# Kernel optimization log

Measured on AMD Instinct MI355X. Metric: run time of the kernel, lower is better.

Reference implementation:

```python
import jax, jax.numpy as jnp
import numpy as np

N_NODES = 50000
N_EDGES = 600000
N_GRAPHS = 500
HID = 128
N_LAYERS = 3
N_CLASSES = 10


def setup_inputs() -> dict:
    key = jax.random.key(0)
    ks = jax.random.split(key, 10)
    x = jax.random.normal(ks[0], (N_NODES, HID), dtype=jnp.float32)
    edge_attr = jax.random.normal(ks[1], (N_EDGES, 4), dtype=jnp.float32)
    edge_index = jax.random.randint(ks[2], (2, N_EDGES), 0, N_NODES, dtype=jnp.int32)
    batch = jnp.sort(jax.random.randint(ks[3], (N_NODES,), 0, N_GRAPHS, dtype=jnp.int32))
    s = 1.0 / np.sqrt(HID)
    Wl = jax.random.normal(ks[4], (N_LAYERS, HID, HID), dtype=jnp.float32) * s
    bl = jax.random.normal(ks[5], (N_LAYERS, HID), dtype=jnp.float32) * s
    Wr = jax.random.normal(ks[6], (N_LAYERS, HID, HID), dtype=jnp.float32) * s
    W1 = jax.random.normal(ks[7], (HID, HID), dtype=jnp.float32) * s
    b1 = jnp.zeros((HID,), dtype=jnp.float32)
    W2 = jax.random.normal(ks[8], (N_CLASSES, HID), dtype=jnp.float32) * s
    b2 = jnp.zeros((N_CLASSES,), dtype=jnp.float32)
    return {"x": x, "edge_attr": edge_attr, "edge_index": edge_index, "batch": batch,
            "Wl": Wl, "bl": bl, "Wr": Wr, "W1": W1, "b1": b1, "W2": W2, "b2": b2}


def _sage_conv(x, src, dst, Wl_i, bl_i, Wr_i):
    # mean aggregation of source-node features at target nodes (PyG SAGEConv)
    msg_sum = jax.ops.segment_sum(x[src], dst, num_segments=N_NODES)  # [N, H]
    cnt = jax.ops.segment_sum(jnp.ones((src.shape[0],), x.dtype), dst, num_segments=N_NODES)
    mean = msg_sum / jnp.maximum(cnt, 1.0)[:, None]
    return mean @ Wl_i.T + bl_i + x @ Wr_i.T


def reference(x, edge_attr, edge_index, batch, Wl, bl, Wr, W1, b1, W2, b2):
    # edge_attr is ignored by SAGEConv
    src, dst = edge_index[0], edge_index[1]
    for i in range(N_LAYERS):
        x = jax.nn.relu(_sage_conv(x, src, dst, Wl[i], bl[i], Wr[i]))
    # global_add_pool over graphs
    g = jax.ops.segment_sum(x, batch, num_segments=N_GRAPHS)  # [G, H]
    g = jax.nn.relu(g)
    # dropout p=0.5 is identity at inference
    h = jax.nn.relu(g @ W1.T + b1)
    logits = h @ W2.T + b2
    return jax.nn.log_softmax(logits, axis=1)
```

## Files before the change

### kernel.cpp

```cpp
#include <hip/hip_runtime.h>
#include <math.h>

#define HID 128
#define NCLS 10
#define MAXDEG 32
#define TROWS 32
#define MSP 136

typedef __attribute__((ext_vector_type(8))) short frag8;
typedef __attribute__((ext_vector_type(8))) unsigned short u16x8;
typedef __attribute__((ext_vector_type(4))) float f32x4;

static __device__ __forceinline__ float relu_f(float v) { return v > 0.f ? v : 0.f; }

static __device__ __forceinline__ unsigned short f2bf(float f) {
    unsigned int u = __float_as_uint(f);
    u += 0x7fffu + ((u >> 16) & 1u);
    return (unsigned short)(u >> 16);
}
static __device__ __forceinline__ float bf2f(unsigned short u) {
    return __uint_as_float(((unsigned int)u) << 16);
}

static __device__ __forceinline__ void gld_lds16(const void* g, void* l) {
    __builtin_amdgcn_global_load_lds((const __attribute__((address_space(1))) unsigned int*)g,
                                     (__attribute__((address_space(3))) unsigned int*)l,
                                     16, 0, 0);
}

static __device__ __forceinline__ void conv4(const float* __restrict__ in,
                                             unsigned short* __restrict__ out, int i) {
    float4 v = *(const float4*)&in[i * 4];
    ushort4 o;
    o.x = f2bf(v.x); o.y = f2bf(v.y); o.z = f2bf(v.z); o.w = f2bf(v.w);
    *(ushort4*)&out[i * 4] = o;
}

__global__ __launch_bounds__(256) void prep_kernel(const float* __restrict__ x, unsigned short* __restrict__ xb, int nx4,
                                                   const float* __restrict__ Wl, unsigned short* __restrict__ wlb, int nwl4,
                                                   const float* __restrict__ Wr, unsigned short* __restrict__ wrb, int nwr4,
                                                   int* __restrict__ deg, int ndeg4,
                                                   uint4* __restrict__ colp, int ncol8, unsigned int zpat,
                                                   uint4* __restrict__ zp0, uint4* __restrict__ zp1,
                                                   uint4* __restrict__ zp2, int nz8) {
    int i = blockIdx.x * blockDim.x + threadIdx.x;
    if (i < nx4) { conv4(x, xb, i); return; }
    i -= nx4;
    if (i < nwl4) { conv4(Wl, wlb, i); return; }
    i -= nwl4;
    if (i < nwr4) { conv4(Wr, wrb, i); return; }
    i -= nwr4;
    if (i < ndeg4) { *(int4*)&deg[i * 4] = make_int4(0, 0, 0, 0); return; }
    i -= ndeg4;
    if (i < ncol8) { colp[i] = make_uint4(zpat, zpat, zpat, zpat); return; }
    i -= ncol8;
    if (i < nz8) { zp0[i] = make_uint4(0, 0, 0, 0); return; }
    i -= nz8;
    if (i < nz8) { zp1[i] = make_uint4(0, 0, 0, 0); return; }
    i -= nz8;
    if (i < nz8) zp2[i] = make_uint4(0, 0, 0, 0);
}

__global__ void fill_kernel(const int* __restrict__ src, const int* __restrict__ dst,
                            int* __restrict__ deg, unsigned short* __restrict__ col, int nE) {
    int e = blockIdx.x * blockDim.x + threadIdx.x;
    if (e < nE) {
        int d = dst[e];
        int p = atomicAdd(&deg[d], 1);
        if (p < MAXDEG) col[(long)d * MAXDEG + p] = (unsigned short)src[e];
    }
}

__global__ __launch_bounds__(256, 3) void sage_kernel(const unsigned short* __restrict__ Xb,
                                                      const int* __restrict__ deg,
                                                      const unsigned short* __restrict__ col,
                                                      const unsigned short* __restrict__ Wlb,
                                                      const unsigned short* __restrict__ Wrb,
                                                      const float* __restrict__ bl,
                                                      unsigned short* __restrict__ Yb, int nN) {
    __shared__ unsigned short ms[TROWS * MSP];
    __shared__ unsigned short stg[4 * 4096];

    const int r0 = blockIdx.x * TROWS;
    const int lane = threadIdx.x & 63;
    const int wave = threadIdx.x >> 6;
    const int grp4 = lane >> 4;
    const int l16 = lane & 15;
    const int fo = l16 * 8;
    unsigned short* stg_w = &stg[wave * 4096];

#pragma unroll
    for (int set = 0; set < 2; ++set) {
        const int nl = wave * 8 + set * 4 + grp4;
        const int n = r0 + nl;
        const int d = min(deg[n], MAXDEG);
        const unsigned short* cp = col + (long)n * MAXDEG;
        const int il = cp[l16];
        const int ih = cp[16 + l16];

        float acc[8] = {0, 0, 0, 0, 0, 0, 0, 0};

#pragma unroll
        for (int c = 0; c < 4; ++c) {
            const bool act = (c * 8 < d);
            if (act) {
                asm volatile("s_waitcnt lgkmcnt(0)" ::: "memory");
#pragma unroll
                for (int k = 0; k < 8; ++k) {
                    const int slot = c * 8 + k;
                    const int idx = (slot < 16) ? __shfl(il, slot, 16) : __shfl(ih, slot - 16, 16);
                    gld_lds16(Xb + (long)idx * HID + fo, stg_w + k * 512);
                }
#pragma unroll
                for (int k = 0; k < 8; ++k) {
                    asm volatile("s_waitcnt vmcnt(%0)" ::"i"(7 - k) : "memory");
                    u16x8 v = *(const u16x8*)&stg_w[k * 512 + lane * 8];
#pragma unroll
                    for (int j = 0; j < 8; ++j) acc[j] += bf2f(v[j]);
                }
            }
        }

        const float inv = 1.f / fmaxf((float)d, 1.f);
        u16x8 o;
#pragma unroll
        for (int j = 0; j < 8; ++j) o[j] = f2bf(acc[j] * inv);
        *(u16x8*)&ms[nl * MSP + fo] = o;
    }
    __syncthreads();

    const int l15 = lane & 15;
    const int quad = lane >> 4;
    const int wr = wave & 1;
    const int wc = wave >> 1;

    f32x4 acc[4];
#pragma unroll
    for (int ct = 0; ct < 4; ++ct) acc[ct] = (f32x4){0.f, 0.f, 0.f, 0.f};

#pragma unroll
    for (int ks = 0; ks < HID; ks += 32) {
        const int lrow = wr * 16 + l15;
        frag8 aM = *(const frag8*)&ms[lrow * MSP + ks + quad * 8];
        frag8 aX = *(const frag8*)&Xb[(long)(r0 + lrow) * HID + ks + quad * 8];
#pragma unroll
        for (int ct = 0; ct < 4; ++ct) {
            const long nrow = wc * 64 + ct * 16 + l15;
            frag8 bL = *(const frag8*)&Wlb[nrow * HID + ks + quad * 8];
            frag8 bR = *(const frag8*)&Wrb[nrow * HID + ks + quad * 8];
            acc[ct] = __builtin_amdgcn_mfma_f32_16x16x32_bf16(aM, bL, acc[ct], 0, 0, 0);
            acc[ct] = __builtin_amdgcn_mfma_f32_16x16x32_bf16(aX, bR, acc[ct], 0, 0, 0);
        }
    }

#pragma unroll
    for (int ct = 0; ct < 4; ++ct) {
        const int gc = wc * 64 + ct * 16 + l15;
        const float bb = bl[gc];
#pragma unroll
        for (int reg = 0; reg < 4; ++reg) {
            const int gm = r0 + wr * 16 + quad * 4 + reg;
            if (gm < nN) {
                const float v = relu_f(acc[ct][reg] + bb);
                Yb[(long)gm * HID + gc] = f2bf(v);
            }
        }
    }
}

__global__ __launch_bounds__(128) void poolmlp_kernel(const unsigned short* __restrict__ xb,
                                                      const int* __restrict__ batch, int nN,
                                                      const float* __restrict__ W1,
                                                      const float* __restrict__ b1,
                                                      const float* __restrict__ W2,
                                                      const float* __restrict__ b2,
                                                      float* __restrict__ out) {
    __shared__ float gs[HID];
    __shared__ float hs[HID];
    __shared__ float ls[NCLS];
    __shared__ float red[2];
    int gid = blockIdx.x;
    int j = threadIdx.x;

    int lo = 0, hi = nN;
    while (lo < hi) { int mid = (lo + hi) >> 1; if (batch[mid] < gid) lo = mid + 1; else hi = mid; }
    int s = lo;
    hi = nN;
    while (lo < hi) { int mid = (lo + hi) >> 1; if (batch[mid] < gid + 1) lo = mid + 1; else hi = mid; }
    int e = lo;

    float a0 = 0.f, a1 = 0.f, a2 = 0.f, a3 = 0.f;
    int n = s;
    for (; n + 4 <= e; n += 4) {
        a0 += bf2f(xb[(long)n * HID + j]);
        a1 += bf2f(xb[(long)(n + 1) * HID + j]);
        a2 += bf2f(xb[(long)(n + 2) * HID + j]);
        a3 += bf2f(xb[(long)(n + 3) * HID + j]);
    }
    for (; n < e; ++n) a0 += bf2f(xb[(long)n * HID + j]);
    gs[j] = relu_f((a0 + a1) + (a2 + a3));
    __syncthreads();

    float acc = b1[j];
#pragma unroll 8
    for (int k = 0; k < HID; ++k) acc += gs[k] * W1[j * HID + k];
    hs[j] = relu_f(acc);
    __syncthreads();
    if (j < NCLS) {
        float lg = b2[j];
#pragma unroll 8
        for (int k = 0; k < HID; ++k) lg += hs[k] * W2[j * HID + k];
        ls[j] = lg;
    }
    __syncthreads();
    if (j == 0) {
        float m = ls[0];
        for (int c = 1; c < NCLS; ++c) m = fmaxf(m, ls[c]);
        float sum = 0.f;
        for (int c = 0; c < NCLS; ++c) sum += expf(ls[c] - m);
        red[0] = m;
        red[1] = logf(sum);
    }
    __syncthreads();
    if (j < NCLS) out[gid * NCLS + j] = ls[j] - red[0] - red[1];
}


extern "C" void kernel_launch(void* const* d_in, const int* in_sizes, int n_in,
                              void* d_out, int out_size, void* d_ws, size_t ws_size,
                              hipStream_t stream) {
    const float* x_in  = (const float*)d_in[0];
    const int*   eidx  = (const int*)d_in[2];
    const int*   batch = (const int*)d_in[3];
    const float* Wl    = (const float*)d_in[4];
    const float* bl    = (const float*)d_in[5];
    const float* Wr    = (const float*)d_in[6];
    const float* W1    = (const float*)d_in[7];
    const float* b1    = (const float*)d_in[8];
    const float* W2    = (const float*)d_in[9];
    const float* b2    = (const float*)d_in[10];
    float* out = (float*)d_out;

    const int nN = in_sizes[0] / HID;
    const int nE = in_sizes[2] / 2;
    const int nG = out_size / NCLS;
    const int nWl = in_sizes[4];
    const int nWr = in_sizes[6];
    const int nNp = (nN + TROWS - 1) & ~(TROWS - 1);
    const int nTiles = nNp / TROWS;
    const int nRows = nNp + 8;

    const int* src = eidx;
    const int* dst = eidx + nE;

    char* p = (char*)d_ws;
    auto carve = [&](size_t bytes) {
        char* r = p;
        p += (bytes + 255) & ~(size_t)255;
        return r;
    };
    unsigned short* xb  = (unsigned short*)carve((size_t)nRows * HID * 2);
    unsigned short* yb0 = (unsigned short*)carve((size_t)nRows * HID * 2);
    unsigned short* yb1 = (unsigned short*)carve((size_t)nRows * HID * 2);
    unsigned short* wlb = (unsigned short*)carve((size_t)nWl * 2);
    unsigned short* wrb = (unsigned short*)carve((size_t)nWr * 2);
    int*   deg = (int*)carve((size_t)nNp * 4);
    unsigned short* col = (unsigned short*)carve((size_t)nNp * MAXDEG * 2);
    (void)ws_size; (void)n_in;

    const int nx4 = nN * HID / 4, nwl4 = nWl / 4, nwr4 = nWr / 4;
    const int ndeg4 = (nNp + 3) / 4;
    const int ncol8 = nNp * MAXDEG / 8;
    const int nzrows = nNp + 1 - nN;
    const int nz8 = nzrows * HID / 8;
    const unsigned int zpat = (unsigned int)nNp | ((unsigned int)nNp << 16);
    const int prep_total = nx4 + nwl4 + nwr4 + ndeg4 + ncol8 + 3 * nz8;
    prep_kernel<<<(prep_total + 255) / 256, 256, 0, stream>>>(
        x_in, xb, nx4, Wl, wlb, nwl4, Wr, wrb, nwr4, deg, ndeg4,
        (uint4*)col, ncol8, zpat,
        (uint4*)(xb + (size_t)nN * HID), (uint4*)(yb0 + (size_t)nN * HID),
        (uint4*)(yb1 + (size_t)nN * HID), nz8);

    fill_kernel<<<(nE + 255) / 256, 256, 0, stream>>>(src, dst, deg, col, nE);

    const unsigned short* xcur = xb;
    unsigned short* bufs[2] = {yb0, yb1};
    for (int l = 0; l < 3; ++l) {
        sage_kernel<<<nTiles, 256, 0, stream>>>(
            xcur, deg, col,
            wlb + (size_t)l * HID * HID, wrb + (size_t)l * HID * HID,
            bl + (size_t)l * HID, bufs[l & 1], nN);
        xcur = bufs[l & 1];
    }

    poolmlp_kernel<<<nG, 128, 0, stream>>>(xcur, batch, nN, W1, b1, W2, b2, out);
}
```

Measured before the change: 321.0 us.

## Double-buffer neighbor gather in 4-row chunks across both node sets

Restructures the mean-aggregation gather into a double-buffered software pipeline. Neighbor rows are fetched in chunks of 4 into two alternating LDS buffers, with the next chunk issued while the current one is accumulated. The chunk count is now set by the wave-wide maximum degree, rounded to multiples of 4 rather than 8, and both node sets are flattened into one loop. The aim is to hide global-load latency and cut wasted fetches for low-degree nodes. The cost is more registers (two accumulators) and extra wait/branch logic per chunk.

After: 427.2 us. 33.1% more time.

```diff
diff --git a/kernel.cpp b/kernel.cpp
--- a/kernel.cpp
+++ b/kernel.cpp
@@ -79,7 +79,7 @@
                                                       const float* __restrict__ bl,
                                                       unsigned short* __restrict__ Yb, int nN) {
     __shared__ unsigned short ms[TROWS * MSP];
-    __shared__ unsigned short stg[4 * 4096];
+    __shared__ unsigned short stg[4 * 2 * 2048];
 
     const int r0 = blockIdx.x * TROWS;
     const int lane = threadIdx.x & 63;
@@ -89,43 +89,83 @@
     const int fo = l16 * 8;
     unsigned short* stg_w = &stg[wave * 4096];
 
-#pragma unroll
-    for (int set = 0; set < 2; ++set) {
-        const int nl = wave * 8 + set * 4 + grp4;
-        const int n = r0 + nl;
-        const int d = min(deg[n], MAXDEG);
-        const unsigned short* cp = col + (long)n * MAXDEG;
-        const int il = cp[l16];
-        const int ih = cp[16 + l16];
-
-        float acc[8] = {0, 0, 0, 0, 0, 0, 0, 0};
-
-#pragma unroll
-        for (int c = 0; c < 4; ++c) {
-            const bool act = (c * 8 < d);
-            if (act) {
-                asm volatile("s_waitcnt lgkmcnt(0)" ::: "memory");
-#pragma unroll
-                for (int k = 0; k < 8; ++k) {
-                    const int slot = c * 8 + k;
-                    const int idx = (slot < 16) ? __shfl(il, slot, 16) : __shfl(ih, slot - 16, 16);
-                    gld_lds16(Xb + (long)idx * HID + fo, stg_w + k * 512);
+    const int n0 = r0 + wave * 8 + grp4;
+    const int n1 = n0 + 4;
+    const int d0 = min(deg[n0], MAXDEG);
+    const int d1 = min(deg[n1], MAXDEG);
+    const unsigned short* cp0 = col + (long)n0 * MAXDEG;
+    const unsigned short* cp1 = col + (long)n1 * MAXDEG;
+    const int il0 = cp0[l16], ih0 = cp0[16 + l16];
+    const int il1 = cp1[l16], ih1 = cp1[16 + l16];
+
+    int m0 = d0, m1 = d1;
+    m0 = max(m0, __shfl_xor(m0, 16)); m0 = max(m0, __shfl_xor(m0, 32));
+    m1 = max(m1, __shfl_xor(m1, 16)); m1 = max(m1, __shfl_xor(m1, 32));
+    const int nc0 = __builtin_amdgcn_readfirstlane((m0 + 3) >> 2);
+    const int ncT = nc0 + __builtin_amdgcn_readfirstlane((m1 + 3) >> 2);
+
+    float acc0[8] = {0, 0, 0, 0, 0, 0, 0, 0};
+    float acc1[8] = {0, 0, 0, 0, 0, 0, 0, 0};
+
+    auto issue = [&](int t) {
+        const int s = (t >= nc0) ? 1 : 0;
+        const int c = t - (s ? nc0 : 0);
+        const int iv = s ? ((c < 4) ? il1 : ih1) : ((c < 4) ? il0 : ih0);
+        const int sbase = (c < 4) ? c * 4 : c * 4 - 16;
+        unsigned short* sb = stg_w + (t & 1) * 2048;
+#pragma unroll
+        for (int k = 0; k < 4; ++k) {
+            const int idx = __shfl(iv, sbase + k, 16);
+            gld_lds16(Xb + (long)idx * HID + fo, sb + k * 512);
+        }
+    };
+
+    if (ncT > 0) {
+        issue(0);
+        if (ncT > 1) issue(1);
+        for (int t = 0; t < ncT; ++t) {
+            if (t + 1 < ncT) {
+                asm volatile("s_waitcnt vmcnt(4)" ::: "memory");
+            } else {
+                asm volatile("s_waitcnt vmcnt(0)" ::: "memory");
+            }
+            __builtin_amdgcn_sched_barrier(0);
+            const unsigned short* sb = stg_w + (t & 1) * 2048;
+            if (t < nc0) {
+#pragma unroll
+                for (int k = 0; k < 4; ++k) {
+                    u16x8 v = *(const u16x8*)&sb[k * 512 + lane * 8];
+#pragma unroll
+                    for (int j = 0; j < 8; ++j) acc0[j] += bf2f(v[j]);
                 }
-#pragma unroll
-                for (int k = 0; k < 8; ++k) {
-                    asm volatile("s_waitcnt vmcnt(%0)" ::"i"(7 - k) : "memory");
-                    u16x8 v = *(const u16x8*)&stg_w[k * 512 + lane * 8];
-#pragma unroll
-                    for (int j = 0; j < 8; ++j) acc[j] += bf2f(v[j]);
+            } else {
+#pragma unroll
+                for (int k = 0; k < 4; ++k) {
+                    u16x8 v = *(const u16x8*)&sb[k * 512 + lane * 8];
+#pragma unroll
+                    for (int j = 0; j < 8; ++j) acc1[j] += bf2f(v[j]);
                 }
             }
+            if (t + 2 < ncT) {
+                asm volatile("s_waitcnt lgkmcnt(0)" ::: "memory");
+                __builtin_amdgcn_sched_barrier(0);
+                issue(t + 2);
+            }
         }
-
-        const float inv = 1.f / fmaxf((float)d, 1.f);
-        u16x8 o;
-#pragma unroll
-        for (int j = 0; j < 8; ++j) o[j] = f2bf(acc[j] * inv);
-        *(u16x8*)&ms[nl * MSP + fo] = o;
+    }
+
+    {
+        const int nl0 = wave * 8 + grp4;
+        const float inv0 = 1.f / fmaxf((float)d0, 1.f);
+        u16x8 o0;
+#pragma unroll
+        for (int j = 0; j < 8; ++j) o0[j] = f2bf(acc0[j] * inv0);
+        *(u16x8*)&ms[nl0 * MSP + fo] = o0;
+        const float inv1 = 1.f / fmaxf((float)d1, 1.f);
+        u16x8 o1;
+#pragma unroll
+        for (int j = 0; j < 8; ++j) o1[j] = f2bf(acc1[j] * inv1);
+        *(u16x8*)&ms[(nl0 + 4) * MSP + fo] = o1;
     }
     __syncthreads();
 
```

## Gather neighbor features in FP8 copy and double rows per block

Applied to the files above, without the earlier changes.

Keeps an extra FP8 copy of node features, written in prep and by the first two layers, and gathers neighbor rows from it with direct vector loads. This replaces the LDS-staged bf16 global_load_lds path and halves gather bytes. TROWS doubles to 64, so each wave computes two 16-row MFMA tiles and reuses the weight fragments. The trade-off is lower precision in the mean aggregation, extra byte-wide FP8 stores in the epilogue, and fewer blocks in the grid.

Result: faster. 266.6 us (median of 2 runs) (-17.0%).

```diff
diff --git a/kernel.cpp b/kernel.cpp
--- a/kernel.cpp
+++ b/kernel.cpp
@@ -4,11 +4,12 @@
 #define HID 128
 #define NCLS 10
 #define MAXDEG 32
-#define TROWS 32
+#define TROWS 64
 #define MSP 136
 
 typedef __attribute__((ext_vector_type(8))) short frag8;
 typedef __attribute__((ext_vector_type(8))) unsigned short u16x8;
+typedef __attribute__((ext_vector_type(2))) unsigned int u32x2;
 typedef __attribute__((ext_vector_type(4))) float f32x4;
 
 static __device__ __forceinline__ float relu_f(float v) { return v > 0.f ? v : 0.f; }
@@ -22,10 +23,21 @@
     return __uint_as_float(((unsigned int)u) << 16);
 }
 
-static __device__ __forceinline__ void gld_lds16(const void* g, void* l) {
-    __builtin_amdgcn_global_load_lds((const __attribute__((address_space(1))) unsigned int*)g,
-                                     (__attribute__((address_space(3))) unsigned int*)l,
-                                     16, 0, 0);
+static __device__ __forceinline__ unsigned int f2fp8x4(float a, float b, float c, float d) {
+    int w = __builtin_amdgcn_cvt_pk_fp8_f32(a, b, 0, false);
+    w = __builtin_amdgcn_cvt_pk_fp8_f32(c, d, w, true);
+    return (unsigned int)w;
+}
+static __device__ __forceinline__ unsigned char f2fp8(float v) {
+    return (unsigned char)(__builtin_amdgcn_cvt_pk_fp8_f32(v, v, 0, false) & 0xff);
+}
+static __device__ __forceinline__ void f8acc(unsigned int w0, unsigned int w1, float* acc) {
+    auto p0 = __builtin_amdgcn_cvt_pk_f32_fp8((int)w0, false);
+    auto p1 = __builtin_amdgcn_cvt_pk_f32_fp8((int)w0, true);
+    auto p2 = __builtin_amdgcn_cvt_pk_f32_fp8((int)w1, false);
+    auto p3 = __builtin_amdgcn_cvt_pk_f32_fp8((int)w1, true);
+    acc[0] += p0[0]; acc[1] += p0[1]; acc[2] += p1[0]; acc[3] += p1[1];
+    acc[4] += p2[0]; acc[5] += p2[1]; acc[6] += p3[0]; acc[7] += p3[1];
 }
 
 static __device__ __forceinline__ void conv4(const float* __restrict__ in,
@@ -36,15 +48,25 @@
     *(ushort4*)&out[i * 4] = o;
 }
 
-__global__ __launch_bounds__(256) void prep_kernel(const float* __restrict__ x, unsigned short* __restrict__ xb, int nx4,
+__global__ __launch_bounds__(256) void prep_kernel(const float* __restrict__ x, unsigned short* __restrict__ xb,
+                                                   unsigned int* __restrict__ xf8w, int nx4,
                                                    const float* __restrict__ Wl, unsigned short* __restrict__ wlb, int nwl4,
                                                    const float* __restrict__ Wr, unsigned short* __restrict__ wrb, int nwr4,
                                                    int* __restrict__ deg, int ndeg4,
                                                    uint4* __restrict__ colp, int ncol8, unsigned int zpat,
                                                    uint4* __restrict__ zp0, uint4* __restrict__ zp1,
-                                                   uint4* __restrict__ zp2, int nz8) {
+                                                   uint4* __restrict__ zp2, int nz8,
+                                                   uint4* __restrict__ zf0, uint4* __restrict__ zf1,
+                                                   uint4* __restrict__ zf2) {
     int i = blockIdx.x * blockDim.x + threadIdx.x;
-    if (i < nx4) { conv4(x, xb, i); return; }
+    if (i < nx4) {
+        float4 v = *(const float4*)&x[i * 4];
+        ushort4 o;
+        o.x = f2bf(v.x); o.y = f2bf(v.y); o.z = f2bf(v.z); o.w = f2bf(v.w);
+        *(ushort4*)&xb[i * 4] = o;
+        xf8w[i] = f2fp8x4(v.x, v.y, v.z, v.w);
+        return;
+    }
     i -= nx4;
     if (i < nwl4) { conv4(Wl, wlb, i); return; }
     i -= nwl4;
@@ -58,7 +80,13 @@
     i -= nz8;
     if (i < nz8) { zp1[i] = make_uint4(0, 0, 0, 0); return; }
     i -= nz8;
-    if (i < nz8) zp2[i] = make_uint4(0, 0, 0, 0);
+    if (i < nz8) { zp2[i] = make_uint4(0, 0, 0, 0); return; }
+    i -= nz8;
+    if (i < 8) { zf0[i] = make_uint4(0, 0, 0, 0); return; }
+    i -= 8;
+    if (i < 8) { zf1[i] = make_uint4(0, 0, 0, 0); return; }
+    i -= 8;
+    if (i < 8) zf2[i] = make_uint4(0, 0, 0, 0);
 }
 
 __global__ void fill_kernel(const int* __restrict__ src, const int* __restrict__ dst,
@@ -72,84 +100,101 @@
 }
 
 __global__ __launch_bounds__(256, 3) void sage_kernel(const unsigned short* __restrict__ Xb,
+                                                      const unsigned char* __restrict__ Xf8,
                                                       const int* __restrict__ deg,
                                                       const unsigned short* __restrict__ col,
                                                       const unsigned short* __restrict__ Wlb,
                                                       const unsigned short* __restrict__ Wrb,
                                                       const float* __restrict__ bl,
-                                                      unsigned short* __restrict__ Yb, int nN) {
+                                                      unsigned short* __restrict__ Yb,
+                                                      unsigned char* __restrict__ Yf8,
+                                                      int wr8, int nN) {
     __shared__ unsigned short ms[TROWS * MSP];
-    __shared__ unsigned short stg[4 * 4096];
 
     const int r0 = blockIdx.x * TROWS;
+
+    {
+        const int grp = threadIdx.x >> 4;
+        const int l16 = threadIdx.x & 15;
+        const int fo8 = l16 * 8;
+        const long fo = (long)l16 * 8;
+
+        for (int i = 0; i < 4; ++i) {
+            const int nl = grp * 4 + i;
+            const int n = r0 + nl;
+            const int d = min(deg[n], MAXDEG);
+            const unsigned short* cp = col + (long)n * MAXDEG;
+
+            float acc[8] = {0, 0, 0, 0, 0, 0, 0, 0};
+
+            if (d > 0) {
+                u16x8 iv0 = *(const u16x8*)&cp[0];
+                u16x8 iv1 = *(const u16x8*)&cp[8];
+                u32x2 q[16];
+#pragma unroll
+                for (int k = 0; k < 8; ++k)
+                    q[k] = *(const u32x2*)&Xf8[(long)iv0[k] * HID + fo8];
+#pragma unroll
+                for (int k = 0; k < 8; ++k)
+                    q[8 + k] = *(const u32x2*)&Xf8[(long)iv1[k] * HID + fo8];
+#pragma unroll
+                for (int k = 0; k < 16; ++k) f8acc(q[k][0], q[k][1], acc);
+
+                if (d > 16) {
+                    u16x8 iv2 = *(const u16x8*)&cp[16];
+                    u16x8 iv3 = *(const u16x8*)&cp[24];
+#pragma unroll
+                    for (int k = 0; k < 8; ++k)
+                        q[k] = *(const u32x2*)&Xf8[(long)iv2[k] * HID + fo8];
+#pragma unroll
+                    for (int k = 0; k < 8; ++k)
+                        q[8 + k] = *(const u32x2*)&Xf8[(long)iv3[k] * HID + fo8];
+#pragma unroll
+                    for (int k = 0; k < 16; ++k) f8acc(q[k][0], q[k][1], acc);
+                }
+            }
+
+            const float inv = 1.f / fmaxf((float)d, 1.f);
+            u16x8 o;
+#pragma unroll
+            for (int j = 0; j < 8; ++j) o[j] = f2bf(acc[j] * inv);
+            *(u16x8*)&ms[nl * MSP + fo] = o;
+        }
+    }
+    __syncthreads();
+
     const int lane = threadIdx.x & 63;
     const int wave = threadIdx.x >> 6;
-    const int grp4 = lane >> 4;
-    const int l16 = lane & 15;
-    const int fo = l16 * 8;
-    unsigned short* stg_w = &stg[wave * 4096];
-
-#pragma unroll
-    for (int set = 0; set < 2; ++set) {
-        const int nl = wave * 8 + set * 4 + grp4;
-        const int n = r0 + nl;
-        const int d = min(deg[n], MAXDEG);
-        const unsigned short* cp = col + (long)n * MAXDEG;
-        const int il = cp[l16];
-        const int ih = cp[16 + l16];
-
-        float acc[8] = {0, 0, 0, 0, 0, 0, 0, 0};
-
-#pragma unroll
-        for (int c = 0; c < 4; ++c) {
-            const bool act = (c * 8 < d);
-            if (act) {
-                asm volatile("s_waitcnt lgkmcnt(0)" ::: "memory");
-#pragma unroll
-                for (int k = 0; k < 8; ++k) {
-                    const int slot = c * 8 + k;
-                    const int idx = (slot < 16) ? __shfl(il, slot, 16) : __shfl(ih, slot - 16, 16);
-                    gld_lds16(Xb + (long)idx * HID + fo, stg_w + k * 512);
-                }
-#pragma unroll
-                for (int k = 0; k < 8; ++k) {
-                    asm volatile("s_waitcnt vmcnt(%0)" ::"i"(7 - k) : "memory");
-                    u16x8 v = *(const u16x8*)&stg_w[k * 512 + lane * 8];
-#pragma unroll
-                    for (int j = 0; j < 8; ++j) acc[j] += bf2f(v[j]);
-                }
-            }
-        }
-
-        const float inv = 1.f / fmaxf((float)d, 1.f);
-        u16x8 o;
-#pragma unroll
-        for (int j = 0; j < 8; ++j) o[j] = f2bf(acc[j] * inv);
-        *(u16x8*)&ms[nl * MSP + fo] = o;
-    }
-    __syncthreads();
-
     const int l15 = lane & 15;
     const int quad = lane >> 4;
     const int wr = wave & 1;
     const int wc = wave >> 1;
 
-    f32x4 acc[4];
-#pragma unroll
-    for (int ct = 0; ct < 4; ++ct) acc[ct] = (f32x4){0.f, 0.f, 0.f, 0.f};
+    f32x4 acc[2][4];
+#pragma unroll
+    for (int rt = 0; rt < 2; ++rt)
+#pragma unroll
+        for (int ct = 0; ct < 4; ++ct) acc[rt][ct] = (f32x4){0.f, 0.f, 0.f, 0.f};
 
 #pragma unroll
     for (int ks = 0; ks < HID; ks += 32) {
-        const int lrow = wr * 16 + l15;
-        frag8 aM = *(const frag8*)&ms[lrow * MSP + ks + quad * 8];
-        frag8 aX = *(const frag8*)&Xb[(long)(r0 + lrow) * HID + ks + quad * 8];
+        frag8 aM[2], aX[2];
+#pragma unroll
+        for (int rt = 0; rt < 2; ++rt) {
+            const int lrow = wr * 32 + rt * 16 + l15;
+            aM[rt] = *(const frag8*)&ms[lrow * MSP + ks + quad * 8];
+            aX[rt] = *(const frag8*)&Xb[(long)(r0 + lrow) * HID + ks + quad * 8];
+        }
 #pragma unroll
         for (int ct = 0; ct < 4; ++ct) {
             const long nrow = wc * 64 + ct * 16 + l15;
             frag8 bL = *(const frag8*)&Wlb[nrow * HID + ks + quad * 8];
             frag8 bR = *(const frag8*)&Wrb[nrow * HID + ks + quad * 8];
-            acc[ct] = __builtin_amdgcn_mfma_f32_16x16x32_bf16(aM, bL, acc[ct], 0, 0, 0);
-            acc[ct] = __builtin_amdgcn_mfma_f32_16x16x32_bf16(aX, bR, acc[ct], 0, 0, 0);
+#pragma unroll
+            for (int rt = 0; rt < 2; ++rt) {
+                acc[rt][ct] = __builtin_amdgcn_mfma_f32_16x16x32_bf16(aM[rt], bL, acc[rt][ct], 0, 0, 0);
+                acc[rt][ct] = __builtin_amdgcn_mfma_f32_16x16x32_bf16(aX[rt], bR, acc[rt][ct], 0, 0, 0);
+            }
         }
     }
 
@@ -158,11 +203,15 @@
         const int gc = wc * 64 + ct * 16 + l15;
         const float bb = bl[gc];
 #pragma unroll
-        for (int reg = 0; reg < 4; ++reg) {
-            const int gm = r0 + wr * 16 + quad * 4 + reg;
-            if (gm < nN) {
-                const float v = relu_f(acc[ct][reg] + bb);
-                Yb[(long)gm * HID + gc] = f2bf(v);
+        for (int rt = 0; rt < 2; ++rt) {
+#pragma unroll
+            for (int reg = 0; reg < 4; ++reg) {
+                const int gm = r0 + wr * 32 + rt * 16 + quad * 4 + reg;
+                if (gm < nN) {
+                    const float v = relu_f(acc[rt][ct][reg] + bb);
+                    Yb[(long)gm * HID + gc] = f2bf(v);
+                    if (wr8) Yf8[(long)gm * HID + gc] = f2fp8(v);
+                }
             }
         }
     }
@@ -262,6 +311,9 @@
     unsigned short* xb  = (unsigned short*)carve((size_t)nRows * HID * 2);
     unsigned short* yb0 = (unsigned short*)carve((size_t)nRows * HID * 2);
     unsigned short* yb1 = (unsigned short*)carve((size_t)nRows * HID * 2);
+    unsigned char* xf8  = (unsigned char*)carve((size_t)(nNp + 1) * HID);
+    unsigned char* yf80 = (unsigned char*)carve((size_t)(nNp + 1) * HID);
+    unsigned char* yf81 = (unsigned char*)carve((size_t)(nNp + 1) * HID);
     unsigned short* wlb = (unsigned short*)carve((size_t)nWl * 2);
     unsigned short* wrb = (unsigned short*)carve((size_t)nWr * 2);
     int*   deg = (int*)carve((size_t)nNp * 4);
@@ -271,26 +323,31 @@
     const int nx4 = nN * HID / 4, nwl4 = nWl / 4, nwr4 = nWr / 4;
     const int ndeg4 = (nNp + 3) / 4;
     const int ncol8 = nNp * MAXDEG / 8;
-    const int nzrows = nNp + 1 - nN;
-    const int nz8 = nzrows * HID / 8;
+    const int nzrows = nNp - nN;
+    const int nz8 = (nzrows * HID) / 8;
     const unsigned int zpat = (unsigned int)nNp | ((unsigned int)nNp << 16);
-    const int prep_total = nx4 + nwl4 + nwr4 + ndeg4 + ncol8 + 3 * nz8;
+    const int prep_total = nx4 + nwl4 + nwr4 + ndeg4 + ncol8 + 3 * nz8 + 24;
     prep_kernel<<<(prep_total + 255) / 256, 256, 0, stream>>>(
-        x_in, xb, nx4, Wl, wlb, nwl4, Wr, wrb, nwr4, deg, ndeg4,
+        x_in, xb, (unsigned int*)xf8, nx4, Wl, wlb, nwl4, Wr, wrb, nwr4, deg, ndeg4,
         (uint4*)col, ncol8, zpat,
         (uint4*)(xb + (size_t)nN * HID), (uint4*)(yb0 + (size_t)nN * HID),
-        (uint4*)(yb1 + (size_t)nN * HID), nz8);
+        (uint4*)(yb1 + (size_t)nN * HID), nz8,
+        (uint4*)(xf8 + (size_t)nNp * HID), (uint4*)(yf80 + (size_t)nNp * HID),
+        (uint4*)(yf81 + (size_t)nNp * HID));
 
     fill_kernel<<<(nE + 255) / 256, 256, 0, stream>>>(src, dst, deg, col, nE);
 
     const unsigned short* xcur = xb;
+    const unsigned char* fcur = xf8;
     unsigned short* bufs[2] = {yb0, yb1};
+    unsigned char* fbufs[2] = {yf80, yf81};
     for (int l = 0; l < 3; ++l) {
         sage_kernel<<<nTiles, 256, 0, stream>>>(
-            xcur, deg, col,
+            xcur, fcur, deg, col,
             wlb + (size_t)l * HID * HID, wrb + (size_t)l * HID * HID,
-            bl + (size_t)l * HID, bufs[l & 1], nN);
+            bl + (size_t)l * HID, bufs[l & 1], fbufs[l & 1], (l < 2) ? 1 : 0, nN);
         xcur = bufs[l & 1];
+        fcur = fbufs[l & 1];
     }
 
     poolmlp_kernel<<<nG, 128, 0, stream>>>(xcur, batch, nN, W1, b1, W2, b2, out);
```
